# Kernel tuning notes

Measured on AMD Instinct MI355X. Metric: run time of the kernel, lower is better.

The kernel has to match this reference:

```python
import jax, jax.numpy as jnp
import numpy as np

EPS = 1e-12  # torch F.normalize eps

def _l2norm(v, axis):
    n = jnp.sqrt(jnp.sum(v * v, axis=axis, keepdims=True))
    return v / jnp.maximum(n, EPS)

def setup_inputs() -> dict:
    key = jax.random.key(0)
    k1, k2, k3 = jax.random.split(key, 3)
    N, D, H, W, K = 32, 512, 56, 56, 64
    x = jax.random.normal(k1, (N, D, H, W), dtype=jnp.float32)
    conv_w = jax.random.normal(k2, (K, D), dtype=jnp.float32) * 0.05
    centroids = jax.random.uniform(k3, (K, D), dtype=jnp.float32)
    return {"x": x, "conv_w": conv_w, "centroids": centroids}

def reference(x, conv_w, centroids):
    N, D, H, W = x.shape
    K = centroids.shape[0]
    # descriptor-wise L2 normalization over channel dim
    x = _l2norm(x, axis=1)
    x_flat = x.reshape(N, D, H * W)                      # (N, D, P)
    # 1x1 conv == per-pixel linear map: (K,D) x (N,D,P) -> (N,K,P)
    logits = jnp.einsum('kd,ndp->nkp', conv_w, x_flat)
    soft_assign = jax.nn.softmax(logits, axis=1)         # softmax over clusters
    # vlad[n,k,:] = sum_p a[n,k,p] * (x[n,:,p] - c[k,:])
    #            = (a @ x^T)[n,k,:] - (sum_p a[n,k,p]) * c[k,:]
    agg = jnp.einsum('nkp,ndp->nkd', soft_assign, x_flat)           # (N, K, D)
    a_sum = jnp.sum(soft_assign, axis=2)                            # (N, K)
    vlad = agg - a_sum[:, :, None] * centroids[None, :, :]
    vlad = _l2norm(vlad, axis=2)        # intra-normalization per cluster
    vlad = vlad.reshape(N, K * D)
    vlad = _l2norm(vlad, axis=1)        # global L2 normalization
    return vlad
```

## Files before the change

### kernel.cpp

```cpp
#include <hip/hip_runtime.h>
#include <hip/hip_bf16.h>

typedef unsigned short u16;
typedef unsigned int u32;
typedef __bf16 bf16x8 __attribute__((ext_vector_type(8)));
typedef float f32x4 __attribute__((ext_vector_type(4)));

#define N_ 32
#define D_ 512
#define P_ 3136
#define K_ 64
#define TILES_P 49
#define NDP (D_ * P_)


__device__ __forceinline__ u16 f2bf(float f) {
  u32 u = __float_as_uint(f);
  return (u16)((u + 0x7fffu + ((u >> 16) & 1u)) >> 16);
}
__device__ __forceinline__ u32 pack2(float a, float b) {
  return (u32)f2bf(a) | ((u32)f2bf(b) << 16);
}

__global__ __launch_bounds__(256) void kw_kernel(const float* __restrict__ w,
                                                 u16* __restrict__ wbf) {
  int i = blockIdx.x * 256 + threadIdx.x;
  float4 v = ((const float4*)w)[i];
  ((uint2*)wbf)[i] = make_uint2(pack2(v.x, v.y), pack2(v.z, v.w));
}

__global__ __launch_bounds__(256) void k1_kernel(const float* __restrict__ x,
                                                 const u16* __restrict__ wbf,
                                                 u16* __restrict__ a_ws,
                                                 float* __restrict__ a_sum) {
  __shared__ __align__(16) char xbuf[65536];
  __shared__ float red[4][64];
  __shared__ float invn_s[64];
  u16* X = (u16*)xbuf;
  float (*a_stage)[65] = (float (*)[65])xbuf;

  const int t = threadIdx.x;
  const int lane = t & 63;
  const int w = t >> 6;
  const int c = lane & 15;
  const int q = lane >> 4;
  const int bid = blockIdx.x;
  const int n = bid / TILES_P;
  const int tile = bid - n * TILES_P;
  const int p0 = tile * 64;
  const int rp = w * 16 + c;

  const float* xg = x + (size_t)n * NDP + p0 + c * 4;
  float La[8][4][4];
#pragma unroll
  for (int g = 0; g < 8; ++g) {
    const int dr = g * 64 + w * 16 + q * 4;
#pragma unroll
    for (int i = 0; i < 4; ++i) {
      float4 v4 = *(const float4*)(xg + (size_t)(dr + i) * P_);
      La[g][i][0] = v4.x; La[g][i][1] = v4.y; La[g][i][2] = v4.z; La[g][i][3] = v4.w;
    }
  }
  float ss[4] = {0.f, 0.f, 0.f, 0.f};
#pragma unroll
  for (int g = 0; g < 8; ++g) {
    const int dr = g * 64 + w * 16 + q * 4;
    const int chunk = dr >> 3;
    const int sub = (q & 1) * 8;
#pragma unroll
    for (int j = 0; j < 4; ++j) {
      float v0 = La[g][0][j], v1 = La[g][1][j], v2 = La[g][2][j], v3 = La[g][3][j];
      ss[j] += v0 * v0 + v1 * v1 + v2 * v2 + v3 * v3;
      const int p = c * 4 + j;
      const int byte = p * 1024 + (((chunk ^ (p & 7)) << 4) | sub);
      *(uint2*)(xbuf + byte) = make_uint2(pack2(v0, v1), pack2(v2, v3));
    }
  }
#pragma unroll
  for (int j = 0; j < 4; ++j) {
    ss[j] += __shfl_xor(ss[j], 16);
    ss[j] += __shfl_xor(ss[j], 32);
  }
  if (q == 0) {
#pragma unroll
    for (int j = 0; j < 4; ++j) red[w][c * 4 + j] = ss[j];
  }
  __syncthreads();

  const float sumsq = red[0][rp] + red[1][rp] + red[2][rp] + red[3][rp];
  const float inv_p = 1.f / fmaxf(sqrtf(sumsq), 1e-12f);
  if (q == 0) invn_s[rp] = inv_p;

  f32x4 acc[4];
#pragma unroll
  for (int m = 0; m < 4; ++m) acc[m] = (f32x4){0.f, 0.f, 0.f, 0.f};
  const int ds_base = rp * 1024;
  const int rmask = rp & 7;
  bf16x8 af[4];
#pragma unroll
  for (int m = 0; m < 4; ++m) af[m] = ((const bf16x8*)wbf)[(m * 16 + c) * 64 + q];
#pragma unroll
  for (int s = 0; s < 16; ++s) {
    bf16x8 afn[4];
    if (s < 15) {
#pragma unroll
      for (int m = 0; m < 4; ++m)
        afn[m] = ((const bf16x8*)wbf)[(m * 16 + c) * 64 + (s + 1) * 4 + q];
    }
    bf16x8 bfrag = *(const bf16x8*)(xbuf + ds_base + (((s * 4 + q) ^ rmask) << 4));
#pragma unroll
    for (int m = 0; m < 4; ++m)
      acc[m] = __builtin_amdgcn_mfma_f32_16x16x32_bf16(af[m], bfrag, acc[m], 0, 0, 0);
    if (s < 15) {
#pragma unroll
      for (int m = 0; m < 4; ++m) af[m] = afn[m];
    }
  }

  float sc[4][4];
  float lmax = -3.0e38f;
#pragma unroll
  for (int m = 0; m < 4; ++m)
#pragma unroll
    for (int r = 0; r < 4; ++r) {
      float val = acc[m][r] * inv_p;
      sc[m][r] = val;
      lmax = fmaxf(lmax, val);
    }
  lmax = fmaxf(lmax, __shfl_xor(lmax, 16));
  lmax = fmaxf(lmax, __shfl_xor(lmax, 32));
  float lsum = 0.f;
#pragma unroll
  for (int m = 0; m < 4; ++m)
#pragma unroll
    for (int r = 0; r < 4; ++r) {
      float e = __expf(sc[m][r] - lmax);
      sc[m][r] = e;
      lsum += e;
    }
  lsum += __shfl_xor(lsum, 16);
  lsum += __shfl_xor(lsum, 32);
  const float rs = 1.f / lsum;

  __syncthreads();
#pragma unroll
  for (int m = 0; m < 4; ++m)
#pragma unroll
    for (int r = 0; r < 4; ++r)
      a_stage[m * 16 + q * 4 + r][rp] = sc[m][r] * rs;
  __syncthreads();

  {
    const int k = t >> 2, pc = t & 3;
    float ssum = 0.f;
    u32 u[8];
#pragma unroll
    for (int jj = 0; jj < 8; ++jj) {
      int p = pc * 16 + jj * 2;
      float a0 = a_stage[k][p], a1 = a_stage[k][p + 1];
      ssum += a0 + a1;
      u[jj] = (u32)f2bf(a0 * invn_s[p]) | ((u32)f2bf(a1 * invn_s[p + 1]) << 16);
    }
    u16* dst = a_ws + (size_t)n * (K_ * P_) + k * P_ + p0 + pc * 16;
    ((uint4*)dst)[0] = make_uint4(u[0], u[1], u[2], u[3]);
    ((uint4*)dst)[1] = make_uint4(u[4], u[5], u[6], u[7]);
    ssum += __shfl_xor(ssum, 1);
    ssum += __shfl_xor(ssum, 2);
    if ((t & 3) == 0) atomicAdd(&a_sum[n * 64 + k], ssum);
  }
}

__global__ __launch_bounds__(256) void k2_kernel(const float* __restrict__ x,
                                                 const u16* __restrict__ a_ws,
                                                 float* __restrict__ agg) {
  int bid = blockIdx.x;
  bid = (bid & 7) * 224 + (bid >> 3);
  const int n = bid / 56;
  const int rem = bid - n * 56;
  const int dblk = rem / 7;
  const int pp = rem - dblk * 7;
  const int t = threadIdx.x;
  const int lane = t & 63, w = t >> 6;
  const int c = lane & 15, q = lane >> 4;
  const int d0 = dblk * 64 + w * 16;

  f32x4 acc[4];
#pragma unroll
  for (int m = 0; m < 4; ++m) acc[m] = (f32x4){0.f, 0.f, 0.f, 0.f};

  const bf16x8* arow = (const bf16x8*)(a_ws + (size_t)n * (K_ * P_));
  const float4* xf = (const float4*)(x + ((size_t)n * D_ + d0 + c) * P_);
  const int it0 = pp * 14;

  float4 pb[2][2];
  bf16x8 pa[2][4];
#pragma unroll
  for (int k2 = 0; k2 < 2; ++k2) {
    pb[k2][0] = xf[(it0 + k2) * 8 + q * 2];
    pb[k2][1] = xf[(it0 + k2) * 8 + q * 2 + 1];
#pragma unroll
    for (int m = 0; m < 4; ++m)
      pa[k2][m] = arow[(m * 16 + c) * 392 + (it0 + k2) * 4 + q];
  }
#pragma unroll
  for (int ii = 0; ii < 14; ++ii) {
    const int cur = ii & 1;
    float4 b0 = pb[cur][0], b1 = pb[cur][1];
    bf16x8 a0_ = pa[cur][0], a1_ = pa[cur][1], a2_ = pa[cur][2], a3_ = pa[cur][3];
    if (ii < 12) {
      pb[cur][0] = xf[(it0 + ii + 2) * 8 + q * 2];
      pb[cur][1] = xf[(it0 + ii + 2) * 8 + q * 2 + 1];
#pragma unroll
      for (int m = 0; m < 4; ++m)
        pa[cur][m] = arow[(m * 16 + c) * 392 + (it0 + ii + 2) * 4 + q];
    }
    bf16x8 bfrag;
    bfrag[0] = (__bf16)b0.x; bfrag[1] = (__bf16)b0.y;
    bfrag[2] = (__bf16)b0.z; bfrag[3] = (__bf16)b0.w;
    bfrag[4] = (__bf16)b1.x; bfrag[5] = (__bf16)b1.y;
    bfrag[6] = (__bf16)b1.z; bfrag[7] = (__bf16)b1.w;
    acc[0] = __builtin_amdgcn_mfma_f32_16x16x32_bf16(a0_, bfrag, acc[0], 0, 0, 0);
    acc[1] = __builtin_amdgcn_mfma_f32_16x16x32_bf16(a1_, bfrag, acc[1], 0, 0, 0);
    acc[2] = __builtin_amdgcn_mfma_f32_16x16x32_bf16(a2_, bfrag, acc[2], 0, 0, 0);
    acc[3] = __builtin_amdgcn_mfma_f32_16x16x32_bf16(a3_, bfrag, acc[3], 0, 0, 0);
  }
  float* ob = agg + ((size_t)pp * 32 + n) * (K_ * D_);
#pragma unroll
  for (int m = 0; m < 4; ++m)
#pragma unroll
    for (int r = 0; r < 4; ++r)
      ob[(m * 16 + q * 4 + r) * D_ + d0 + c] = acc[m][r];
}

__global__ __launch_bounds__(64) void k3a_kernel(const float* __restrict__ agg,
                                                 const float* __restrict__ a_sum,
                                                 const float* __restrict__ cent,
                                                 float* __restrict__ out,
                                                 float* __restrict__ rowsq) {
  const int b = blockIdx.x;
  const int n = b >> 6, k = b & 63;
  const int t = threadIdx.x;
  const float* ab = agg + ((size_t)n * 64 + k) * 512 + t * 8;
  float v[8];
#pragma unroll
  for (int j = 0; j < 8; ++j) v[j] = 0.f;
#pragma unroll
  for (int pp = 0; pp < 7; ++pp) {
    const float4* p4 = (const float4*)(ab + (size_t)pp * 32 * (K_ * D_));
    float4 r0 = p4[0], r1 = p4[1];
    v[0] += r0.x; v[1] += r0.y; v[2] += r0.z; v[3] += r0.w;
    v[4] += r1.x; v[5] += r1.y; v[6] += r1.z; v[7] += r1.w;
  }
  const float asum = a_sum[b];
  const float4* c4 = (const float4*)(cent + k * 512 + t * 8);
  float4 c0 = c4[0], c1 = c4[1];
  v[0] -= asum * c0.x; v[1] -= asum * c0.y; v[2] -= asum * c0.z; v[3] -= asum * c0.w;
  v[4] -= asum * c1.x; v[5] -= asum * c1.y; v[6] -= asum * c1.z; v[7] -= asum * c1.w;
  float ssq = 0.f;
#pragma unroll
  for (int j = 0; j < 8; ++j) ssq += v[j] * v[j];
  ssq += __shfl_xor(ssq, 1);  ssq += __shfl_xor(ssq, 2);  ssq += __shfl_xor(ssq, 4);
  ssq += __shfl_xor(ssq, 8);  ssq += __shfl_xor(ssq, 16); ssq += __shfl_xor(ssq, 32);
  float4* o4 = (float4*)(out + (size_t)n * 32768 + k * 512 + t * 8);
  o4[0] = make_float4(v[0], v[1], v[2], v[3]);
  o4[1] = make_float4(v[4], v[5], v[6], v[7]);
  if (t == 0) rowsq[b] = ssq;
}

__global__ __launch_bounds__(256) void k3b_kernel(const float* __restrict__ rowsq,
                                                  float* __restrict__ out) {
  __shared__ float invr_s[64];
  __shared__ float gi_s;
  const int n = blockIdx.x >> 3;
  const int seg = blockIdx.x & 7;
  const int t = threadIdx.x;
  if (t < 64) {
    float r = rowsq[n * 64 + t];
    float ri = 1.f / fmaxf(sqrtf(r), 1e-12f);
    invr_s[t] = ri;
    float g = r * ri * ri;
    g += __shfl_xor(g, 1); g += __shfl_xor(g, 2); g += __shfl_xor(g, 4);
    g += __shfl_xor(g, 8); g += __shfl_xor(g, 16); g += __shfl_xor(g, 32);
    if (t == 0) gi_s = 1.f / fmaxf(sqrtf(g), 1e-12f);
  }
  __syncthreads();
  const int e0 = seg * 4096 + t * 16;
  const float sc = invr_s[e0 >> 9] * gi_s;
  float4* o4 = (float4*)(out + (size_t)n * 32768 + e0);
#pragma unroll
  for (int i = 0; i < 4; ++i) {
    float4 vv = o4[i];
    vv.x *= sc; vv.y *= sc; vv.z *= sc; vv.w *= sc;
    o4[i] = vv;
  }
}

extern "C" void kernel_launch(void* const* d_in, const int* in_sizes, int n_in,
                              void* d_out, int out_size, void* d_ws, size_t ws_size,
                              hipStream_t stream) {
  (void)in_sizes; (void)n_in; (void)out_size; (void)ws_size;
  const float* x    = (const float*)d_in[0];
  const float* cw   = (const float*)d_in[1];
  const float* cent = (const float*)d_in[2];
  float* out = (float*)d_out;
  char* ws = (char*)d_ws;
  u16*   wbf   = (u16*)(ws);
  u16*   a_ws  = (u16*)(ws + 65536);
  float* a_sum = (float*)(ws + 12910592);
  float* agg   = (float*)(ws + 12918784);
  float* rowsq = (float*)(ws + 42278912);

  hipMemsetAsync(a_sum, 0, 64 * 32 * sizeof(float), stream);
  kw_kernel<<<32, 256, 0, stream>>>(cw, wbf);
  k1_kernel<<<32 * TILES_P, 256, 0, stream>>>(x, wbf, a_ws, a_sum);
  k2_kernel<<<1792, 256, 0, stream>>>(x, a_ws, agg);
  k3a_kernel<<<2048, 64, 0, stream>>>(agg, a_sum, cent, out, rowsq);
  k3b_kernel<<<256, 256, 0, stream>>>(rowsq, out);
}
```

Baseline: 403.2 us.

## Coalesce x loads in k1/k2 via row-wise float4 reads and LDS staging

k2 now loads its x tile row-wise with coalesced float4 reads, converts it to bf16 into a padded LDS buffer, and feeds the MFMA B operand from LDS. Before, each lane read scattered strided columns of x straight from global memory. k1's x load is restructured to read 8 consecutive channels per thread with double-buffered prefetch and 16-byte LDS stores. Both kernels now prefetch weight and assignment fragments two steps ahead and declare an occupancy hint of 2 blocks per CU. The block index remapping in k2 also changes, which affects L2 locality.

```diff
diff --git a/kernel.cpp b/kernel.cpp
--- a/kernel.cpp
+++ b/kernel.cpp
@@ -29,14 +29,13 @@
   ((uint2*)wbf)[i] = make_uint2(pack2(v.x, v.y), pack2(v.z, v.w));
 }
 
-__global__ __launch_bounds__(256) void k1_kernel(const float* __restrict__ x,
-                                                 const u16* __restrict__ wbf,
-                                                 u16* __restrict__ a_ws,
-                                                 float* __restrict__ a_sum) {
+__global__ __launch_bounds__(256, 2) void k1_kernel(const float* __restrict__ x,
+                                                    const u16* __restrict__ wbf,
+                                                    u16* __restrict__ a_ws,
+                                                    float* __restrict__ a_sum) {
   __shared__ __align__(16) char xbuf[65536];
   __shared__ float red[4][64];
   __shared__ float invn_s[64];
-  u16* X = (u16*)xbuf;
   float (*a_stage)[65] = (float (*)[65])xbuf;
 
   const int t = threadIdx.x;
@@ -51,29 +50,31 @@
   const int rp = w * 16 + c;
 
   const float* xg = x + (size_t)n * NDP + p0 + c * 4;
-  float La[8][4][4];
-#pragma unroll
-  for (int g = 0; g < 8; ++g) {
-    const int dr = g * 64 + w * 16 + q * 4;
-#pragma unroll
-    for (int i = 0; i < 4; ++i) {
-      float4 v4 = *(const float4*)(xg + (size_t)(dr + i) * P_);
-      La[g][i][0] = v4.x; La[g][i][1] = v4.y; La[g][i][2] = v4.z; La[g][i][3] = v4.w;
-    }
-  }
+  const int cb = w * 4 + q;
+  float4 L[2][8];
   float ss[4] = {0.f, 0.f, 0.f, 0.f};
 #pragma unroll
-  for (int g = 0; g < 8; ++g) {
-    const int dr = g * 64 + w * 16 + q * 4;
-    const int chunk = dr >> 3;
-    const int sub = (q & 1) * 8;
+  for (int e = 0; e < 8; ++e)
+    L[0][e] = *(const float4*)(xg + (size_t)(cb * 8 + e) * P_);
+#pragma unroll
+  for (int g = 0; g < 4; ++g) {
+    const int cg = g * 16 + cb;
+    if (g < 3) {
+#pragma unroll
+      for (int e = 0; e < 8; ++e)
+        L[(g + 1) & 1][e] = *(const float4*)(xg + (size_t)((cg + 16) * 8 + e) * P_);
+    }
+    const float* Bf = (const float*)&L[g & 1][0];
 #pragma unroll
     for (int j = 0; j < 4; ++j) {
-      float v0 = La[g][0][j], v1 = La[g][1][j], v2 = La[g][2][j], v3 = La[g][3][j];
-      ss[j] += v0 * v0 + v1 * v1 + v2 * v2 + v3 * v3;
+      const float v0 = Bf[0 * 4 + j], v1 = Bf[1 * 4 + j], v2 = Bf[2 * 4 + j],
+                  v3 = Bf[3 * 4 + j], v4 = Bf[4 * 4 + j], v5 = Bf[5 * 4 + j],
+                  v6 = Bf[6 * 4 + j], v7 = Bf[7 * 4 + j];
+      ss[j] += v0 * v0 + v1 * v1 + v2 * v2 + v3 * v3 +
+               v4 * v4 + v5 * v5 + v6 * v6 + v7 * v7;
       const int p = c * 4 + j;
-      const int byte = p * 1024 + (((chunk ^ (p & 7)) << 4) | sub);
-      *(uint2*)(xbuf + byte) = make_uint2(pack2(v0, v1), pack2(v2, v3));
+      *(uint4*)(xbuf + p * 1024 + ((cg ^ (p & 7)) << 4)) =
+          make_uint4(pack2(v0, v1), pack2(v2, v3), pack2(v4, v5), pack2(v6, v7));
     }
   }
 #pragma unroll
@@ -96,24 +97,27 @@
   for (int m = 0; m < 4; ++m) acc[m] = (f32x4){0.f, 0.f, 0.f, 0.f};
   const int ds_base = rp * 1024;
   const int rmask = rp & 7;
-  bf16x8 af[4];
-#pragma unroll
-  for (int m = 0; m < 4; ++m) af[m] = ((const bf16x8*)wbf)[(m * 16 + c) * 64 + q];
+  bf16x8 af[2][4];
+#pragma unroll
+  for (int m = 0; m < 4; ++m) {
+    af[0][m] = ((const bf16x8*)wbf)[(m * 16 + c) * 64 + q];
+    af[1][m] = ((const bf16x8*)wbf)[(m * 16 + c) * 64 + 4 + q];
+  }
 #pragma unroll
   for (int s = 0; s < 16; ++s) {
-    bf16x8 afn[4];
-    if (s < 15) {
+    bf16x8 bfrag = *(const bf16x8*)(xbuf + ds_base + (((s * 4 + q) ^ rmask) << 4));
+    bf16x8 nf[4];
+    if (s < 14) {
 #pragma unroll
       for (int m = 0; m < 4; ++m)
-        afn[m] = ((const bf16x8*)wbf)[(m * 16 + c) * 64 + (s + 1) * 4 + q];
-    }
-    bf16x8 bfrag = *(const bf16x8*)(xbuf + ds_base + (((s * 4 + q) ^ rmask) << 4));
+        nf[m] = ((const bf16x8*)wbf)[(m * 16 + c) * 64 + (s + 2) * 4 + q];
+    }
 #pragma unroll
     for (int m = 0; m < 4; ++m)
-      acc[m] = __builtin_amdgcn_mfma_f32_16x16x32_bf16(af[m], bfrag, acc[m], 0, 0, 0);
-    if (s < 15) {
-#pragma unroll
-      for (int m = 0; m < 4; ++m) af[m] = afn[m];
+      acc[m] = __builtin_amdgcn_mfma_f32_16x16x32_bf16(af[s & 1][m], bfrag, acc[m], 0, 0, 0);
+    if (s < 14) {
+#pragma unroll
+      for (int m = 0; m < 4; ++m) af[s & 1][m] = nf[m];
     }
   }
 
@@ -170,59 +174,73 @@
   }
 }
 
-__global__ __launch_bounds__(256) void k2_kernel(const float* __restrict__ x,
-                                                 const u16* __restrict__ a_ws,
-                                                 float* __restrict__ agg) {
-  int bid = blockIdx.x;
-  bid = (bid & 7) * 224 + (bid >> 3);
-  const int n = bid / 56;
-  const int rem = bid - n * 56;
-  const int dblk = rem / 7;
-  const int pp = rem - dblk * 7;
+__global__ __launch_bounds__(256, 2) void k2_kernel(const float* __restrict__ x,
+                                                    const u16* __restrict__ a_ws,
+                                                    float* __restrict__ agg) {
+  __shared__ __align__(16) char xs[64 * 912];
+  const int b = blockIdx.x;
+  const int dblk = (b >> 3) & 7;
+  const int gidx = (b & 7) * 28 + (b >> 6);
+  const int n = gidx / 7;
+  const int pp = gidx - n * 7;
   const int t = threadIdx.x;
   const int lane = t & 63, w = t >> 6;
   const int c = lane & 15, q = lane >> 4;
+  const int slot = w * 4 + q;
+
+  const float* xrow = x + ((size_t)n * D_ + dblk * 64) * P_ + pp * 448 + c * 4;
+  float4 Lr[2][7];
+#pragma unroll
+  for (int e = 0; e < 7; ++e)
+    Lr[0][e] = *(const float4*)(xrow + (size_t)slot * P_ + e * 64);
+#pragma unroll
+  for (int j = 0; j < 4; ++j) {
+    if (j < 3) {
+#pragma unroll
+      for (int e = 0; e < 7; ++e)
+        Lr[(j + 1) & 1][e] = *(const float4*)(xrow + (size_t)((j + 1) * 16 + slot) * P_ + e * 64);
+    }
+    const int row = j * 16 + slot;
+    char* wb = xs + row * 912 + c * 8;
+    const float* Bf = (const float*)&Lr[j & 1][0];
+#pragma unroll
+    for (int e = 0; e < 7; ++e)
+      *(uint2*)(wb + e * 128) =
+          make_uint2(pack2(Bf[e * 4 + 0], Bf[e * 4 + 1]),
+                     pack2(Bf[e * 4 + 2], Bf[e * 4 + 3]));
+  }
+  __syncthreads();
+
   const int d0 = dblk * 64 + w * 16;
-
+  const u16* abase = a_ws + (size_t)n * (K_ * P_) + pp * 448;
   f32x4 acc[4];
 #pragma unroll
   for (int m = 0; m < 4; ++m) acc[m] = (f32x4){0.f, 0.f, 0.f, 0.f};
-
-  const bf16x8* arow = (const bf16x8*)(a_ws + (size_t)n * (K_ * P_));
-  const float4* xf = (const float4*)(x + ((size_t)n * D_ + d0 + c) * P_);
-  const int it0 = pp * 14;
-
-  float4 pb[2][2];
   bf16x8 pa[2][4];
 #pragma unroll
-  for (int k2 = 0; k2 < 2; ++k2) {
-    pb[k2][0] = xf[(it0 + k2) * 8 + q * 2];
-    pb[k2][1] = xf[(it0 + k2) * 8 + q * 2 + 1];
+  for (int m = 0; m < 4; ++m) {
+    pa[0][m] = *(const bf16x8*)(abase + (size_t)(m * 16 + c) * P_ + q * 8);
+    pa[1][m] = *(const bf16x8*)(abase + (size_t)(m * 16 + c) * P_ + 32 + q * 8);
+  }
+  const char* bbase = xs + (w * 16 + c) * 912 + q * 16;
+  bf16x8 bf0 = *(const bf16x8*)bbase;
+#pragma unroll
+  for (int it = 0; it < 14; ++it) {
+    bf16x8 bcur = bf0;
+    if (it < 13) bf0 = *(const bf16x8*)(bbase + (it + 1) * 64);
+    bf16x8 na[4];
+    if (it < 12) {
+#pragma unroll
+      for (int m = 0; m < 4; ++m)
+        na[m] = *(const bf16x8*)(abase + (size_t)(m * 16 + c) * P_ + (it + 2) * 32 + q * 8);
+    }
 #pragma unroll
     for (int m = 0; m < 4; ++m)
-      pa[k2][m] = arow[(m * 16 + c) * 392 + (it0 + k2) * 4 + q];
-  }
-#pragma unroll
-  for (int ii = 0; ii < 14; ++ii) {
-    const int cur = ii & 1;
-    float4 b0 = pb[cur][0], b1 = pb[cur][1];
-    bf16x8 a0_ = pa[cur][0], a1_ = pa[cur][1], a2_ = pa[cur][2], a3_ = pa[cur][3];
-    if (ii < 12) {
-      pb[cur][0] = xf[(it0 + ii + 2) * 8 + q * 2];
-      pb[cur][1] = xf[(it0 + ii + 2) * 8 + q * 2 + 1];
-#pragma unroll
-      for (int m = 0; m < 4; ++m)
-        pa[cur][m] = arow[(m * 16 + c) * 392 + (it0 + ii + 2) * 4 + q];
-    }
-    bf16x8 bfrag;
-    bfrag[0] = (__bf16)b0.x; bfrag[1] = (__bf16)b0.y;
-    bfrag[2] = (__bf16)b0.z; bfrag[3] = (__bf16)b0.w;
-    bfrag[4] = (__bf16)b1.x; bfrag[5] = (__bf16)b1.y;
-    bfrag[6] = (__bf16)b1.z; bfrag[7] = (__bf16)b1.w;
-    acc[0] = __builtin_amdgcn_mfma_f32_16x16x32_bf16(a0_, bfrag, acc[0], 0, 0, 0);
-    acc[1] = __builtin_amdgcn_mfma_f32_16x16x32_bf16(a1_, bfrag, acc[1], 0, 0, 0);
-    acc[2] = __builtin_amdgcn_mfma_f32_16x16x32_bf16(a2_, bfrag, acc[2], 0, 0, 0);
-    acc[3] = __builtin_amdgcn_mfma_f32_16x16x32_bf16(a3_, bfrag, acc[3], 0, 0, 0);
+      acc[m] = __builtin_amdgcn_mfma_f32_16x16x32_bf16(pa[it & 1][m], bcur, acc[m], 0, 0, 0);
+    if (it < 12) {
+#pragma unroll
+      for (int m = 0; m < 4; ++m) pa[it & 1][m] = na[m];
+    }
   }
   float* ob = agg + ((size_t)pp * 32 + n) * (K_ * D_);
 #pragma unroll
```

Result: no change. 409.7 us (+1.6%).
